# Performance work log

Measured on AMD Instinct MI355X. Metric: run time of the kernel, lower is better.

## Reference

```python
import jax, jax.numpy as jnp
import numpy as np

# --- hyperparameters (from MambaBlock init) ---
DIM = 256          # d_model per window
STEP = 128         # int(dim * hop), hop = 0.5
N_MAMBA = 2
D_STATE = 16
D_CONV = 4
EXPAND = 4
D_INNER = EXPAND * DIM          # 1024
DT_RANK = -(-DIM // 16)         # ceil(d_model/16) = 16
EPS = 1e-5
B_SZ = 4
T_LEN = 131072


def setup_inputs() -> dict:
    key = jax.random.key(0)
    ks = jax.random.split(key, 8)
    s = 0.02
    x = jax.random.normal(ks[0], (B_SZ, T_LEN), dtype=jnp.float32)
    in_proj_w = jax.random.normal(ks[1], (N_MAMBA, 2 * D_INNER, DIM), dtype=jnp.float32) * s
    conv_w = jax.random.normal(ks[2], (N_MAMBA, D_INNER, 1, D_CONV), dtype=jnp.float32) * 0.1
    conv_b = jnp.zeros((N_MAMBA, D_INNER), dtype=jnp.float32)
    x_proj_w = jax.random.normal(ks[3], (N_MAMBA, DT_RANK + 2 * D_STATE, D_INNER), dtype=jnp.float32) * s
    dt_std = DT_RANK ** -0.5
    dt_proj_w = jax.random.uniform(ks[4], (N_MAMBA, D_INNER, DT_RANK), minval=-dt_std, maxval=dt_std, dtype=jnp.float32)
    # dt bias: inverse-softplus of dt ~ LogUniform[1e-3, 0.1] (mamba_ssm init)
    dt = jnp.exp(jax.random.uniform(ks[5], (N_MAMBA, D_INNER), dtype=jnp.float32)
                 * (np.log(0.1) - np.log(1e-3)) + np.log(1e-3))
    dt_proj_b = dt + jnp.log(-jnp.expm1(-dt))
    A_log = jnp.log(jnp.broadcast_to(jnp.arange(1, D_STATE + 1, dtype=jnp.float32),
                                     (N_MAMBA, D_INNER, D_STATE)))
    D_param = jnp.ones((N_MAMBA, D_INNER), dtype=jnp.float32)
    out_proj_w = jax.random.normal(ks[6], (N_MAMBA, DIM, D_INNER), dtype=jnp.float32) * s
    norm_w = jnp.ones((N_MAMBA, DIM), dtype=jnp.float32)
    return dict(x=x, in_proj_w=in_proj_w, conv_w=conv_w, conv_b=conv_b,
                x_proj_w=x_proj_w, dt_proj_w=dt_proj_w, dt_proj_b=dt_proj_b,
                A_log=A_log, D_param=D_param, out_proj_w=out_proj_w, norm_w=norm_w)


def _rmsnorm(x, w):
    return x * jax.lax.rsqrt(jnp.mean(x * x, axis=-1, keepdims=True) + EPS) * w


def _selective_scan(u, delta, A, Bm, Cm, Dp):
    # u, delta: [B, L, Di]; A: [Di, N]; Bm, Cm: [B, L, N]; Dp: [Di]
    def step(h, inp):
        u_t, d_t, B_t, C_t = inp                       # [B,Di],[B,Di],[B,N],[B,N]
        dA = jnp.exp(d_t[:, :, None] * A)              # [B,Di,N]
        h = dA * h + (d_t * u_t)[:, :, None] * B_t[:, None, :]
        y_t = jnp.einsum('bdn,bn->bd', h, C_t)
        return h, y_t
    h0 = jnp.zeros((u.shape[0], u.shape[2], A.shape[1]), u.dtype)
    xs = (u.transpose(1, 0, 2), delta.transpose(1, 0, 2),
          Bm.transpose(1, 0, 2), Cm.transpose(1, 0, 2))
    _, ys = jax.lax.scan(step, h0, xs)                 # ys: [L, B, Di]
    return ys.transpose(1, 0, 2) + u * Dp


def _mamba(x, in_w, cw, cb, xp_w, dt_w, dt_b, A_log, Dp, out_w):
    # x: [B, L, d_model]
    xz = jnp.einsum('bld,ed->ble', x, in_w)            # [B, L, 2*Di]
    xc, z = jnp.split(xz, 2, axis=-1)
    # causal depthwise conv (torch pads d_conv-1 both sides then truncates to L)
    xc = xc.transpose(0, 2, 1)                         # [B, Di, L]
    xc = jax.lax.conv_general_dilated(xc, cw, window_strides=(1,),
                                      padding=[(D_CONV - 1, 0)],
                                      feature_group_count=D_INNER,
                                      dimension_numbers=('NCH', 'OIH', 'NCH'))
    xc = jax.nn.silu(xc + cb[None, :, None]).transpose(0, 2, 1)  # [B, L, Di]
    x_dbl = jnp.einsum('bld,ed->ble', xc, xp_w)        # [B, L, dt_rank + 2N]
    dt = x_dbl[..., :DT_RANK]
    Bm = x_dbl[..., DT_RANK:DT_RANK + D_STATE]
    Cm = x_dbl[..., DT_RANK + D_STATE:]
    delta = jax.nn.softplus(jnp.einsum('blr,dr->bld', dt, dt_w) + dt_b)
    A = -jnp.exp(A_log)                                # [Di, N]
    y = _selective_scan(xc, delta, A, Bm, Cm, Dp)
    y = y * jax.nn.silu(z)
    return jnp.einsum('bld,ed->ble', y, out_w)         # [B, L, d_model]


def _forward(x, in_proj_w, conv_w, conv_b, x_proj_w, dt_proj_w, dt_proj_b,
             A_log, D_param, out_proj_w, norm_w):
    B, T = x.shape
    L = (T - DIM) // STEP + 1
    idx = jnp.arange(L)[:, None] * STEP + jnp.arange(DIM)[None, :]  # [L, DIM]
    h = x[:, idx]                                      # unfold -> [B, L, DIM]
    res = None
    for i in range(N_MAMBA):
        res = h + res if res is not None else h        # Block residual chaining
        hn = _rmsnorm(res, norm_w[i])
        h = _mamba(hn, in_proj_w[i], conv_w[i], conv_b[i], x_proj_w[i],
                   dt_proj_w[i], dt_proj_b[i], A_log[i], D_param[i], out_proj_w[i])
    r = h + res
    # hop < 1: triangular window, then fold (overlap-add)
    half = DIM // 2
    win = jnp.concatenate([jnp.linspace(0.0, 1.0, half), jnp.linspace(1.0, 0.0, half)])
    r = r * win
    folded = jnp.zeros_like(x).at[:, idx].add(r)       # F.fold overlap-add
    return folded + x


def reference(x, in_proj_w, conv_w, conv_b, x_proj_w, dt_proj_w, dt_proj_b,
              A_log, D_param, out_proj_w, norm_w):
    return _forward(x, in_proj_w, conv_w, conv_b, x_proj_w, dt_proj_w, dt_proj_b,
                    A_log, D_param, out_proj_w, norm_w)
```

## Files before the change

### kernel.cpp

```cpp
#include <hip/hip_runtime.h>
#include <cmath>

#define DIMC   256
#define L_WIN  1023
#define M_VALID 4092
#define M_PAD  4096
#define DI     1024
#define TLEN   131072
#define SEG    32
#define NSEG   32

typedef __bf16 bf16x8 __attribute__((ext_vector_type(8)));
typedef __bf16 bf16x4 __attribute__((ext_vector_type(4)));
typedef float  f32x4  __attribute__((ext_vector_type(4)));

__device__ __forceinline__ float sigmoidf_(float x){ return 1.f/(1.f + __expf(-x)); }
__device__ __forceinline__ float softplusf_(float v){ return fmaxf(v,0.f) + log1pf(__expf(-fabsf(v))); }

template<int CTRL>
__device__ __forceinline__ float dpp_add(float x){
  int v = __builtin_amdgcn_update_dpp(0, __builtin_bit_cast(int, x), CTRL, 0xF, 0xF, true);
  return x + __builtin_bit_cast(float, v);
}

__global__ __launch_bounds__(256) void init_kernel(const float* __restrict__ x, float* __restrict__ res,
    const float* __restrict__ a, __bf16* __restrict__ da, int na,
    const float* __restrict__ b, __bf16* __restrict__ db, int nb,
    const float* __restrict__ c, __bf16* __restrict__ dc, int nc)
{
  if (blockIdx.x < M_PAD){
    int m = blockIdx.x, j = threadIdx.x;
    float v = 0.f;
    if (m < M_VALID){
      int bb = m / L_WIN, l = m - bb*L_WIN;
      v = x[(size_t)bb*TLEN + l*128 + j];
    }
    res[(size_t)m*DIMC + j] = v;
    return;
  }
  int nblk = gridDim.x - M_PAD;
  int stride = nblk*256;
  int base = (blockIdx.x - M_PAD)*256 + threadIdx.x;
  for (int i = base; i < na; i += stride) da[i] = (__bf16)a[i];
  for (int i = base; i < nb; i += stride) db[i] = (__bf16)b[i];
  for (int i = base; i < nc; i += stride) dc[i] = (__bf16)c[i];
}

__global__ __launch_bounds__(256) void rms_kernel(const float* __restrict__ src, __bf16* __restrict__ dst,
                                                  const float* __restrict__ w){
  int m = blockIdx.x, j = threadIdx.x;
  float v = (m < M_VALID) ? src[(size_t)m*DIMC + j] : 0.f;
  float s = v*v;
  #pragma unroll
  for (int off = 32; off; off >>= 1) s += __shfl_down(s, off);
  __shared__ float ls[4];
  if ((threadIdx.x & 63) == 0) ls[threadIdx.x >> 6] = s;
  __syncthreads();
  float tot = ls[0] + ls[1] + ls[2] + ls[3];
  float scale = rsqrtf(tot * (1.f/DIMC) + 1e-5f);
  dst[(size_t)m*DIMC + j] = (__bf16)(v * scale * w[j]);
}

template<int WM, int WN, typename OutT>
__global__ __launch_bounds__(256) void gemm_tiled_kernel(const __bf16* __restrict__ A, const __bf16* __restrict__ B,
    OutT* C, const float* addsrc, int K, int ldc)
{
  constexpr int BM  = 32*WM;
  constexpr int BN  = 32*WN;
  constexpr int LDK = 72;
  __shared__ __bf16 As[BM*LDK];
  __shared__ __bf16 Bs[BN*LDK];
  int tid  = threadIdx.x;
  int lane = tid & 63, wv = tid >> 6;
  int row  = lane & 15, kq = lane >> 4;
  int m0 = blockIdx.x*BM, n0 = blockIdx.y*BN;
  int wmo = (wv >> 1)*(16*WM);
  int wno = (wv &  1)*(16*WN);
  f32x4 acc[WM][WN] = {};
  for (int kt = 0; kt < K; kt += 64){
    __syncthreads();
    #pragma unroll
    for (int r = 0; r < BM/32; ++r){
      int seg = r*256 + tid;
      int rw = seg >> 3, sb = seg & 7;
      *(bf16x8*)(As + rw*LDK + sb*8) = *(const bf16x8*)(A + (size_t)(m0 + rw)*K + kt + sb*8);
    }
    #pragma unroll
    for (int r = 0; r < BN/32; ++r){
      int seg = r*256 + tid;
      int rw = seg >> 3, sb = seg & 7;
      *(bf16x8*)(Bs + rw*LDK + sb*8) = *(const bf16x8*)(B + (size_t)(n0 + rw)*K + kt + sb*8);
    }
    __syncthreads();
    #pragma unroll
    for (int ks = 0; ks < 2; ++ks){
      bf16x8 af[WM], bfr[WN];
      #pragma unroll
      for (int i = 0; i < WM; ++i) af[i]  = *(const bf16x8*)(As + (wmo + i*16 + row)*LDK + ks*32 + kq*8);
      #pragma unroll
      for (int j = 0; j < WN; ++j) bfr[j] = *(const bf16x8*)(Bs + (wno + j*16 + row)*LDK + ks*32 + kq*8);
      #pragma unroll
      for (int i = 0; i < WM; ++i){
        #pragma unroll
        for (int j = 0; j < WN; ++j)
          acc[i][j] = __builtin_amdgcn_mfma_f32_16x16x32_bf16(af[i], bfr[j], acc[i][j], 0, 0, 0);
      }
    }
  }
  #pragma unroll
  for (int i = 0; i < WM; ++i){
    int cm = m0 + wmo + i*16 + kq*4;
    #pragma unroll
    for (int j = 0; j < WN; ++j){
      int cn = n0 + wno + j*16 + row;
      #pragma unroll
      for (int ii = 0; ii < 4; ++ii){
        size_t idx = (size_t)(cm + ii)*ldc + cn;
        float v = acc[i][j][ii];
        if (addsrc) v += addsrc[idx];
        C[idx] = (OutT)v;
      }
    }
  }
}

template<int SUBN, typename OutT>
__global__ __launch_bounds__(256) void gemm_kernel(const __bf16* __restrict__ A, const __bf16* __restrict__ B,
    OutT* C, const float* addsrc, int K, int ldc)
{
  int lane = threadIdx.x & 63;
  int wv   = threadIdx.x >> 6;
  int row  = lane & 15;
  int kq   = lane >> 4;
  int m0 = blockIdx.x*64 + wv*16;
  int n0 = blockIdx.y*(16*SUBN);
  f32x4 acc[SUBN] = {};
  const __bf16* Ap = A + (size_t)(m0 + row)*K + kq*8;
  const __bf16* Bp = B + (size_t)(n0 + row)*K + kq*8;
  for (int k = 0; k < K; k += 32){
    bf16x8 a = *(const bf16x8*)(Ap + k);
    #pragma unroll
    for (int s = 0; s < SUBN; ++s){
      bf16x8 bb = *(const bf16x8*)(Bp + (size_t)s*16*K + k);
      acc[s] = __builtin_amdgcn_mfma_f32_16x16x32_bf16(a, bb, acc[s], 0, 0, 0);
    }
  }
  int cm = m0 + kq*4;
  #pragma unroll
  for (int s = 0; s < SUBN; ++s){
    int cn = n0 + s*16 + row;
    #pragma unroll
    for (int i = 0; i < 4; ++i){
      size_t idx = (size_t)(cm + i)*ldc + cn;
      float v = acc[s][i];
      if (addsrc) v += addsrc[idx];
      C[idx] = (OutT)v;
    }
  }
}

__global__ __launch_bounds__(256) void conv_kernel(const __bf16* __restrict__ xz16, const float* __restrict__ cw,
    const float* __restrict__ cb, __bf16* __restrict__ u16)
{
  int m0 = blockIdx.x * 16;
  int d  = threadIdx.x * 4;
  float w[4][4];
  #pragma unroll
  for (int c = 0; c < 4; ++c){
    #pragma unroll
    for (int j = 0; j < 4; ++j) w[c][j] = cw[(d + c)*4 + j];
  }
  float bias[4];
  #pragma unroll
  for (int c = 0; c < 4; ++c) bias[c] = cb[d + c];
  for (int ti = 0; ti < 16; ++ti){
    int m = m0 + ti;
    float acc[4] = {0.f, 0.f, 0.f, 0.f};
    if (m < M_VALID){
      int b = m / L_WIN;
      int l = m - b*L_WIN;
      #pragma unroll
      for (int c = 0; c < 4; ++c) acc[c] = bias[c];
      #pragma unroll
      for (int k = 0; k < 4; ++k){
        if (l >= k){
          bf16x4 xv = *(const bf16x4*)(xz16 + (size_t)(m - k)*2048 + d);
          #pragma unroll
          for (int c = 0; c < 4; ++c) acc[c] = fmaf((float)xv[c], w[c][3-k], acc[c]);
        }
      }
      #pragma unroll
      for (int c = 0; c < 4; ++c) acc[c] = acc[c] * sigmoidf_(acc[c]);
    }
    bf16x4 o;
    #pragma unroll
    for (int c = 0; c < 4; ++c) o[c] = (__bf16)acc[c];
    *(bf16x4*)(u16 + (size_t)m*DI + d) = o;
  }
}

__global__ __launch_bounds__(256) void dtproj_kernel(const float* __restrict__ xdbl, const float* __restrict__ dtw,
    const float* __restrict__ dtb, __bf16* __restrict__ delta16)
{
  int m0 = blockIdx.x * 16;
  int tid = threadIdx.x;
  __shared__ float sdt[16][17];
  sdt[tid >> 4][tid & 15] = xdbl[(size_t)(m0 + (tid >> 4))*48 + (tid & 15)];
  __syncthreads();
  int d0 = tid * 4;
  float w[4][16];
  #pragma unroll
  for (int c = 0; c < 4; ++c){
    #pragma unroll
    for (int q = 0; q < 16; ++q) w[c][q] = dtw[(d0 + c)*16 + q];
  }
  float bias[4];
  #pragma unroll
  for (int c = 0; c < 4; ++c) bias[c] = dtb[d0 + c];
  for (int t = 0; t < 16; ++t){
    float acc[4] = {bias[0], bias[1], bias[2], bias[3]};
    #pragma unroll
    for (int r = 0; r < 16; ++r){
      float dv = sdt[t][r];
      #pragma unroll
      for (int c = 0; c < 4; ++c) acc[c] = fmaf(dv, w[c][r], acc[c]);
    }
    bf16x4 o;
    #pragma unroll
    for (int c = 0; c < 4; ++c) o[c] = (__bf16)softplusf_(acc[c]);
    *(bf16x4*)(delta16 + (size_t)(m0 + t)*DI + d0) = o;
  }
}

__global__ __launch_bounds__(256) void scan_part1_kernel(
  const __bf16* __restrict__ u16, const __bf16* __restrict__ delta16,
  const float* __restrict__ xdbl, const float* __restrict__ Alog, float2* __restrict__ Pq)
{
  int bid = blockIdx.x;
  int s = bid & 31, dtile = (bid >> 5) & 63, b = bid >> 11;
  int d0 = dtile << 4;
  int tid = threadIdx.x;
  int c = tid >> 4, n = tid & 15;
  float A_dn = -__expf(Alog[(d0 + c)*16 + n]);
  __shared__ float2 sdd[16][SEG+2];
  __shared__ float  sB [SEG][17];
  int t0 = s*SEG;
  int nt = L_WIN - t0; if (nt > SEG) nt = SEG;
  size_t base_m = (size_t)b*L_WIN + t0;
  for (int i2 = tid; i2 < 16*SEG; i2 += 256){
    int tt = i2 >> 4, dd = i2 & 15;
    float dlt = 0.f, du = 0.f, Bv = 0.f;
    if (tt < nt){
      size_t m = base_m + tt;
      dlt = (float)delta16[m*DI + d0 + dd];
      du  = dlt * (float)u16[m*DI + d0 + dd];
      Bv  = xdbl[m*48 + 16 + dd];
    }
    sdd[dd][tt] = make_float2(dlt, du);
    sB[tt][dd]  = Bv;
  }
  __syncthreads();
  float h = 0.f, P = 1.f;
  #pragma unroll 8
  for (int t = 0; t < SEG; ++t){
    float2 dd2 = sdd[c][t];
    float dA = __expf(dd2.x * A_dn);
    h = fmaf(dA, h, dd2.y * sB[t][n]);
    P *= dA;
  }
  Pq[(((size_t)b*NSEG + s) << 14) + d0*16 + tid] = make_float2(P, h);
}

__global__ __launch_bounds__(256) void scan_combine_kernel(const float2* __restrict__ Pq,
                                                           float* __restrict__ hstart)
{
  int idx = blockIdx.x*256 + threadIdx.x;
  int b = idx >> 14;
  int dn = idx & 16383;
  float hs = 0.f;
  #pragma unroll
  for (int s = 0; s < NSEG; ++s){
    size_t o = (((size_t)b*NSEG + s) << 14) + dn;
    hstart[o] = hs;
    float2 pq = Pq[o];
    hs = fmaf(pq.x, hs, pq.y);
  }
}

__global__ __launch_bounds__(256) void scan_part2_kernel(
  const __bf16* __restrict__ u16, const __bf16* __restrict__ delta16,
  const float* __restrict__ xdbl, const __bf16* __restrict__ xz16,
  const float* __restrict__ Alog, const float* __restrict__ Dp,
  const float* __restrict__ hstart, __bf16* __restrict__ y16)
{
  int bid = blockIdx.x;
  int s = bid & 31, dtile = (bid >> 5) & 63, b = bid >> 11;
  int d0 = dtile << 4;
  int tid = threadIdx.x;
  int c = tid >> 4, n = tid & 15;
  float A_dn = -__expf(Alog[(d0 + c)*16 + n]);
  __shared__ float2 sdd[16][SEG+2];
  __shared__ float2 sBC[SEG][17];
  __shared__ float  sy [16][SEG+1];
  __shared__ float  sD[16];
  if (tid < 16) sD[tid] = Dp[d0 + tid];
  int t0 = s*SEG;
  int nt = L_WIN - t0; if (nt > SEG) nt = SEG;
  size_t base_m = (size_t)b*L_WIN + t0;
  for (int i2 = tid; i2 < 16*SEG; i2 += 256){
    int tt = i2 >> 4, dd = i2 & 15;
    float dlt = 0.f, uu = 0.f, Bv = 0.f, Cv = 0.f;
    if (tt < nt){
      size_t m = base_m + tt;
      dlt = (float)delta16[m*DI + d0 + dd];
      uu  = (float)u16[m*DI + d0 + dd];
      Bv  = xdbl[m*48 + 16 + dd];
      Cv  = xdbl[m*48 + 32 + dd];
    }
    sdd[dd][tt] = make_float2(dlt, uu);
    sBC[tt][dd] = make_float2(Bv, Cv);
  }
  float h = hstart[(((size_t)b*NSEG + s) << 14) + d0*16 + tid];
  __syncthreads();
  #pragma unroll 8
  for (int t = 0; t < SEG; ++t){
    float2 dd2 = sdd[c][t];
    float dA = __expf(dd2.x * A_dn);
    float2 bc = sBC[t][n];
    h = fmaf(dA, h, dd2.x * dd2.y * bc.x);
    float pp = h * bc.y;
    pp = dpp_add<0xB1>(pp);
    pp = dpp_add<0x4E>(pp);
    pp = dpp_add<0x141>(pp);
    pp = dpp_add<0x128>(pp);
    if (n == 0) sy[c][t] = pp;
  }
  __syncthreads();
  for (int i2 = tid; i2 < 16*nt; i2 += 256){
    int tt = i2 >> 4, dd = i2 & 15;
    size_t m = base_m + tt;
    float uv = sdd[dd][tt].y;
    float zv = (float)xz16[m*2048 + 1024 + d0 + dd];
    float yv = (sy[dd][tt] + uv * sD[dd]) * (zv * sigmoidf_(zv));
    y16[m*DI + d0 + dd] = (__bf16)yv;
  }
}

__global__ __launch_bounds__(256) void fold_kernel(const float* __restrict__ x, const float* __restrict__ r,
                                                   float* __restrict__ out){
  int i = blockIdx.x*256 + threadIdx.x;
  int b = i >> 17;
  int t = i & (TLEN - 1);
  float acc = x[i];
  int l1 = t >> 7;
  int j  = t & 127;
  if (l1 < L_WIN) acc += r[((size_t)b*L_WIN + l1)*DIMC + j] * ((float)j * (1.f/127.f));
  if (l1 >= 1)    acc += r[((size_t)b*L_WIN + l1 - 1)*DIMC + j + 128] * ((float)(127 - j) * (1.f/127.f));
  out[i] = acc;
}

extern "C" void kernel_launch(void* const* d_in, const int* in_sizes, int n_in,
                              void* d_out, int out_size, void* d_ws, size_t ws_size,
                              hipStream_t stream)
{
  (void)in_sizes; (void)n_in; (void)out_size; (void)ws_size;
  const float* x      = (const float*)d_in[0];
  const float* in_w   = (const float*)d_in[1];
  const float* conv_w = (const float*)d_in[2];
  const float* conv_b = (const float*)d_in[3];
  const float* xp_w   = (const float*)d_in[4];
  const float* dt_w   = (const float*)d_in[5];
  const float* dt_b   = (const float*)d_in[6];
  const float* A_log  = (const float*)d_in[7];
  const float* Dp     = (const float*)d_in[8];
  const float* out_w  = (const float*)d_in[9];
  const float* norm_w = (const float*)d_in[10];
  float* out = (float*)d_out;

  char* p = (char*)d_ws;
  auto alloc = [&](size_t bytes)->void*{ void* r = (void*)p; p += (bytes + 255) & ~(size_t)255; return r; };
  float*  res    = (float*) alloc((size_t)M_PAD*DIMC*4);
  __bf16* hn16   = (__bf16*)alloc((size_t)M_PAD*DIMC*2);
  __bf16* xz16   = (__bf16*)alloc((size_t)M_PAD*2048*2);
  __bf16* u16    = (__bf16*)alloc((size_t)M_PAD*DI*2);
  float*  xdbl   = (float*) alloc((size_t)M_PAD*48*4);
  __bf16* delta16= (__bf16*)alloc((size_t)M_PAD*DI*2);
  __bf16* y16    = (__bf16*)alloc((size_t)M_PAD*DI*2);
  float2* Pq     = (float2*)alloc((size_t)4*NSEG*16384*8);
  float*  hstart = (float*) alloc((size_t)4*NSEG*16384*4);
  __bf16* w_in16 = (__bf16*)alloc((size_t)2*2048*256*2);
  __bf16* w_xp16 = (__bf16*)alloc((size_t)2*48*1024*2);
  __bf16* w_out16= (__bf16*)alloc((size_t)2*256*1024*2);

  init_kernel<<<M_PAD + 512, 256, 0, stream>>>(x, res,
                                               in_w, w_in16, 2*2048*256,
                                               xp_w, w_xp16, 2*48*1024,
                                               out_w, w_out16, 2*256*1024);

  for (int i = 0; i < 2; ++i){
    rms_kernel<<<M_PAD, 256, 0, stream>>>(res, hn16, norm_w + i*256);
    gemm_tiled_kernel<4, 4, __bf16><<<dim3(32, 16), 256, 0, stream>>>(hn16, w_in16 + (size_t)i*524288, xz16, nullptr, 256, 2048);
    conv_kernel<<<M_PAD/16, 256, 0, stream>>>(xz16, conv_w + i*4096, conv_b + i*1024, u16);
    gemm_kernel<1, float><<<dim3(64, 3), 256, 0, stream>>>(u16, w_xp16 + (size_t)i*49152, xdbl, nullptr, 1024, 48);
    dtproj_kernel<<<M_PAD/16, 256, 0, stream>>>(xdbl, dt_w + i*16384, dt_b + i*1024, delta16);
    scan_part1_kernel<<<8192, 256, 0, stream>>>(u16, delta16, xdbl, A_log + i*16384, Pq);
    scan_combine_kernel<<<256, 256, 0, stream>>>(Pq, hstart);
    scan_part2_kernel<<<8192, 256, 0, stream>>>(u16, delta16, xdbl, xz16, A_log + i*16384, Dp + i*1024,
                                                hstart, y16);
    gemm_tiled_kernel<2, 2, float><<<dim3(64, 4), 256, 0, stream>>>(y16, w_out16 + (size_t)i*262144, res, res, 1024, 256);
  }
  fold_kernel<<<TLEN*4/256, 256, 0, stream>>>(x, res, out);
}
```

Measured before the change: 357.7 us.

## Fuse dt projection and three-pass selective scan into one block-per-chain kernel

Replaces the dt projection kernel and the three scan kernels (part1, combine, part2) with a single kernel. Each 1024-thread block owns one (batch, 16-channel) chain and walks the 32 segments in 8 rounds of 4, combining segment carries in shared memory. This removes the delta16, Pq and hstart global round-trips and three launches. The cost is that only 256 blocks run each scan, with sequential rounds and many barriers, so parallelism drops sharply compared with 8192 independent blocks. Delta and u are also now held at different precision (fp32 delta, bf16 u in shared memory).

```diff
diff --git a/kernel.cpp b/kernel.cpp
--- a/kernel.cpp
+++ b/kernel.cpp
@@ -9,6 +9,7 @@
 #define TLEN   131072
 #define SEG    32
 #define NSEG   32
+#define ROUNDS 8
 
 typedef __bf16 bf16x8 __attribute__((ext_vector_type(8)));
 typedef __bf16 bf16x4 __attribute__((ext_vector_type(4)));
@@ -199,150 +200,108 @@
   }
 }
 
-__global__ __launch_bounds__(256) void dtproj_kernel(const float* __restrict__ xdbl, const float* __restrict__ dtw,
-    const float* __restrict__ dtb, __bf16* __restrict__ delta16)
-{
-  int m0 = blockIdx.x * 16;
+__global__ __launch_bounds__(1024) void scan_fused_kernel(
+  const __bf16* __restrict__ u16, const float* __restrict__ xdbl,
+  const __bf16* __restrict__ xz16,
+  const float* __restrict__ dtw, const float* __restrict__ dtb,
+  const float* __restrict__ Alog, const float* __restrict__ Dp,
+  __bf16* __restrict__ y16)
+{
+  int chain = blockIdx.x;
+  int b = chain >> 6;
+  int d0 = (chain & 63) << 4;
   int tid = threadIdx.x;
-  __shared__ float sdt[16][17];
-  sdt[tid >> 4][tid & 15] = xdbl[(size_t)(m0 + (tid >> 4))*48 + (tid & 15)];
-  __syncthreads();
-  int d0 = tid * 4;
-  float w[4][16];
-  #pragma unroll
-  for (int c = 0; c < 4; ++c){
-    #pragma unroll
-    for (int q = 0; q < 16; ++q) w[c][q] = dtw[(d0 + c)*16 + q];
-  }
-  float bias[4];
-  #pragma unroll
-  for (int c = 0; c < 4; ++c) bias[c] = dtb[d0 + c];
-  for (int t = 0; t < 16; ++t){
-    float acc[4] = {bias[0], bias[1], bias[2], bias[3]};
-    #pragma unroll
-    for (int r = 0; r < 16; ++r){
-      float dv = sdt[t][r];
-      #pragma unroll
-      for (int c = 0; c < 4; ++c) acc[c] = fmaf(dv, w[c][r], acc[c]);
-    }
-    bf16x4 o;
-    #pragma unroll
-    for (int c = 0; c < 4; ++c) o[c] = (__bf16)softplusf_(acc[c]);
-    *(bf16x4*)(delta16 + (size_t)(m0 + t)*DI + d0) = o;
-  }
-}
-
-__global__ __launch_bounds__(256) void scan_part1_kernel(
-  const __bf16* __restrict__ u16, const __bf16* __restrict__ delta16,
-  const float* __restrict__ xdbl, const float* __restrict__ Alog, float2* __restrict__ Pq)
-{
-  int bid = blockIdx.x;
-  int s = bid & 31, dtile = (bid >> 5) & 63, b = bid >> 11;
-  int d0 = dtile << 4;
-  int tid = threadIdx.x;
-  int c = tid >> 4, n = tid & 15;
+  int g = tid >> 8;
+  int t256 = tid & 255;
+  int c = t256 >> 4, n = t256 & 15;
   float A_dn = -__expf(Alog[(d0 + c)*16 + n]);
-  __shared__ float2 sdd[16][SEG+2];
-  __shared__ float  sB [SEG][17];
-  int t0 = s*SEG;
-  int nt = L_WIN - t0; if (nt > SEG) nt = SEG;
-  size_t base_m = (size_t)b*L_WIN + t0;
-  for (int i2 = tid; i2 < 16*SEG; i2 += 256){
-    int tt = i2 >> 4, dd = i2 & 15;
-    float dlt = 0.f, du = 0.f, Bv = 0.f;
-    if (tt < nt){
+
+  __shared__ float2 sdd[4][16][SEG+1];
+  __shared__ float2 sBC[4][SEG][17];
+  __shared__ float  sy [4][16][SEG+1];
+  __shared__ __bf16 su [4][16][SEG+2];
+  __shared__ float  sdt[4][SEG][17];
+  __shared__ float2 strans[4][256];
+  __shared__ float  sH[2][256];
+  __shared__ float  sW[16][17];
+  __shared__ float  sbias[16];
+  __shared__ float  sD[16];
+
+  if (tid < 256){
+    sW[c][n] = dtw[(size_t)(d0 + c)*16 + n];
+    sH[0][t256] = 0.f;
+    if (tid < 16){ sbias[tid] = dtb[d0 + tid]; sD[tid] = Dp[d0 + tid]; }
+  }
+
+  for (int r = 0; r < ROUNDS; ++r){
+    int s = r*4 + g;
+    int t0 = s*SEG;
+    int nt = L_WIN - t0; if (nt > SEG) nt = SEG;
+    size_t base_m = (size_t)b*L_WIN + t0;
+    __syncthreads();
+    for (int i2 = t256; i2 < 16*SEG; i2 += 256){
+      int tt = i2 >> 4, k = i2 & 15;
+      float dtv = 0.f, Bv = 0.f, Cv = 0.f, uu = 0.f;
+      if (tt < nt){
+        const float* rowp = xdbl + (base_m + tt)*48;
+        dtv = rowp[k]; Bv = rowp[16 + k]; Cv = rowp[32 + k];
+        uu  = (float)u16[(base_m + tt)*DI + d0 + k];
+      }
+      sdt[g][tt][k] = dtv;
+      sBC[g][tt][k] = make_float2(Bv, Cv);
+      su[g][k][tt]  = (__bf16)uu;
+    }
+    __syncthreads();
+    for (int i2 = t256; i2 < 16*SEG; i2 += 256){
+      int tt = i2 >> 4, dd = i2 & 15;
+      float acc = sbias[dd];
+      #pragma unroll
+      for (int rr = 0; rr < 16; ++rr) acc = fmaf(sdt[g][tt][rr], sW[dd][rr], acc);
+      float dlt = softplusf_(acc);
+      float uu = (float)su[g][dd][tt];
+      sdd[g][dd][tt] = make_float2(dlt, dlt * uu);
+    }
+    __syncthreads();
+    float h = 0.f, P = 1.f;
+    #pragma unroll 8
+    for (int t = 0; t < SEG; ++t){
+      float2 d2 = sdd[g][c][t];
+      float dA = __expf(d2.x * A_dn);
+      h = fmaf(dA, h, d2.y * sBC[g][t][n].x);
+      P *= dA;
+    }
+    strans[g][t256] = make_float2(P, h);
+    __syncthreads();
+    int par = r & 1;
+    float hs = sH[par][t256];
+    #pragma unroll
+    for (int k = 0; k < 3; ++k){
+      if (k < g){ float2 tr = strans[k][t256]; hs = fmaf(tr.x, hs, tr.y); }
+    }
+    if (g == 3){ float2 tr = strans[3][t256]; sH[par ^ 1][t256] = fmaf(tr.x, hs, tr.y); }
+    h = hs;
+    #pragma unroll 8
+    for (int t = 0; t < SEG; ++t){
+      float2 d2 = sdd[g][c][t];
+      float dA = __expf(d2.x * A_dn);
+      float2 bc = sBC[g][t][n];
+      h = fmaf(dA, h, d2.y * bc.x);
+      float pp = h * bc.y;
+      pp = dpp_add<0xB1>(pp);
+      pp = dpp_add<0x4E>(pp);
+      pp = dpp_add<0x141>(pp);
+      pp = dpp_add<0x128>(pp);
+      if (n == 0) sy[g][c][t] = pp;
+    }
+    __syncthreads();
+    for (int i2 = t256; i2 < 16*nt; i2 += 256){
+      int tt = i2 >> 4, dd = i2 & 15;
       size_t m = base_m + tt;
-      dlt = (float)delta16[m*DI + d0 + dd];
-      du  = dlt * (float)u16[m*DI + d0 + dd];
-      Bv  = xdbl[m*48 + 16 + dd];
-    }
-    sdd[dd][tt] = make_float2(dlt, du);
-    sB[tt][dd]  = Bv;
-  }
-  __syncthreads();
-  float h = 0.f, P = 1.f;
-  #pragma unroll 8
-  for (int t = 0; t < SEG; ++t){
-    float2 dd2 = sdd[c][t];
-    float dA = __expf(dd2.x * A_dn);
-    h = fmaf(dA, h, dd2.y * sB[t][n]);
-    P *= dA;
-  }
-  Pq[(((size_t)b*NSEG + s) << 14) + d0*16 + tid] = make_float2(P, h);
-}
-
-__global__ __launch_bounds__(256) void scan_combine_kernel(const float2* __restrict__ Pq,
-                                                           float* __restrict__ hstart)
-{
-  int idx = blockIdx.x*256 + threadIdx.x;
-  int b = idx >> 14;
-  int dn = idx & 16383;
-  float hs = 0.f;
-  #pragma unroll
-  for (int s = 0; s < NSEG; ++s){
-    size_t o = (((size_t)b*NSEG + s) << 14) + dn;
-    hstart[o] = hs;
-    float2 pq = Pq[o];
-    hs = fmaf(pq.x, hs, pq.y);
-  }
-}
-
-__global__ __launch_bounds__(256) void scan_part2_kernel(
-  const __bf16* __restrict__ u16, const __bf16* __restrict__ delta16,
-  const float* __restrict__ xdbl, const __bf16* __restrict__ xz16,
-  const float* __restrict__ Alog, const float* __restrict__ Dp,
-  const float* __restrict__ hstart, __bf16* __restrict__ y16)
-{
-  int bid = blockIdx.x;
-  int s = bid & 31, dtile = (bid >> 5) & 63, b = bid >> 11;
-  int d0 = dtile << 4;
-  int tid = threadIdx.x;
-  int c = tid >> 4, n = tid & 15;
-  float A_dn = -__expf(Alog[(d0 + c)*16 + n]);
-  __shared__ float2 sdd[16][SEG+2];
-  __shared__ float2 sBC[SEG][17];
-  __shared__ float  sy [16][SEG+1];
-  __shared__ float  sD[16];
-  if (tid < 16) sD[tid] = Dp[d0 + tid];
-  int t0 = s*SEG;
-  int nt = L_WIN - t0; if (nt > SEG) nt = SEG;
-  size_t base_m = (size_t)b*L_WIN + t0;
-  for (int i2 = tid; i2 < 16*SEG; i2 += 256){
-    int tt = i2 >> 4, dd = i2 & 15;
-    float dlt = 0.f, uu = 0.f, Bv = 0.f, Cv = 0.f;
-    if (tt < nt){
-      size_t m = base_m + tt;
-      dlt = (float)delta16[m*DI + d0 + dd];
-      uu  = (float)u16[m*DI + d0 + dd];
-      Bv  = xdbl[m*48 + 16 + dd];
-      Cv  = xdbl[m*48 + 32 + dd];
-    }
-    sdd[dd][tt] = make_float2(dlt, uu);
-    sBC[tt][dd] = make_float2(Bv, Cv);
-  }
-  float h = hstart[(((size_t)b*NSEG + s) << 14) + d0*16 + tid];
-  __syncthreads();
-  #pragma unroll 8
-  for (int t = 0; t < SEG; ++t){
-    float2 dd2 = sdd[c][t];
-    float dA = __expf(dd2.x * A_dn);
-    float2 bc = sBC[t][n];
-    h = fmaf(dA, h, dd2.x * dd2.y * bc.x);
-    float pp = h * bc.y;
-    pp = dpp_add<0xB1>(pp);
-    pp = dpp_add<0x4E>(pp);
-    pp = dpp_add<0x141>(pp);
-    pp = dpp_add<0x128>(pp);
-    if (n == 0) sy[c][t] = pp;
-  }
-  __syncthreads();
-  for (int i2 = tid; i2 < 16*nt; i2 += 256){
-    int tt = i2 >> 4, dd = i2 & 15;
-    size_t m = base_m + tt;
-    float uv = sdd[dd][tt].y;
-    float zv = (float)xz16[m*2048 + 1024 + d0 + dd];
-    float yv = (sy[dd][tt] + uv * sD[dd]) * (zv * sigmoidf_(zv));
-    y16[m*DI + d0 + dd] = (__bf16)yv;
+      float uv = (float)su[g][dd][tt];
+      float zv = (float)xz16[m*2048 + 1024 + d0 + dd];
+      float yv = (sy[g][dd][tt] + uv * sD[dd]) * (zv * sigmoidf_(zv));
+      y16[m*DI + d0 + dd] = (__bf16)yv;
+    }
   }
 }
 
@@ -384,10 +343,7 @@
   __bf16* xz16   = (__bf16*)alloc((size_t)M_PAD*2048*2);
   __bf16* u16    = (__bf16*)alloc((size_t)M_PAD*DI*2);
   float*  xdbl   = (float*) alloc((size_t)M_PAD*48*4);
-  __bf16* delta16= (__bf16*)alloc((size_t)M_PAD*DI*2);
   __bf16* y16    = (__bf16*)alloc((size_t)M_PAD*DI*2);
-  float2* Pq     = (float2*)alloc((size_t)4*NSEG*16384*8);
-  float*  hstart = (float*) alloc((size_t)4*NSEG*16384*4);
   __bf16* w_in16 = (__bf16*)alloc((size_t)2*2048*256*2);
   __bf16* w_xp16 = (__bf16*)alloc((size_t)2*48*1024*2);
   __bf16* w_out16= (__bf16*)alloc((size_t)2*256*1024*2);
@@ -402,11 +358,8 @@
     gemm_tiled_kernel<4, 4, __bf16><<<dim3(32, 16), 256, 0, stream>>>(hn16, w_in16 + (size_t)i*524288, xz16, nullptr, 256, 2048);
     conv_kernel<<<M_PAD/16, 256, 0, stream>>>(xz16, conv_w + i*4096, conv_b + i*1024, u16);
     gemm_kernel<1, float><<<dim3(64, 3), 256, 0, stream>>>(u16, w_xp16 + (size_t)i*49152, xdbl, nullptr, 1024, 48);
-    dtproj_kernel<<<M_PAD/16, 256, 0, stream>>>(xdbl, dt_w + i*16384, dt_b + i*1024, delta16);
-    scan_part1_kernel<<<8192, 256, 0, stream>>>(u16, delta16, xdbl, A_log + i*16384, Pq);
-    scan_combine_kernel<<<256, 256, 0, stream>>>(Pq, hstart);
-    scan_part2_kernel<<<8192, 256, 0, stream>>>(u16, delta16, xdbl, xz16, A_log + i*16384, Dp + i*1024,
-                                                hstart, y16);
+    scan_fused_kernel<<<256, 1024, 0, stream>>>(u16, xdbl, xz16, dt_w + i*16384, dt_b + i*1024,
+                                                A_log + i*16384, Dp + i*1024, y16);
     gemm_tiled_kernel<2, 2, float><<<dim3(64, 4), 256, 0, stream>>>(y16, w_out16 + (size_t)i*262144, res, res, 1024, 256);
   }
   fold_kernel<<<TLEN*4/256, 256, 0, stream>>>(x, res, out);
```

Measured after the change: 370.7 us. +3.6%, slower.

## Fuse conv, x_proj GEMM and dt_proj into one kernel per token tile

Applied to the files above, without the earlier changes.

Merges the depthwise conv+SiLU, the x_proj GEMM and the dt_proj+softplus into a single kernel working on 16-token tiles. The conv output is staged in shared memory and fed straight to MFMA for x_proj, and the dt rows pass through shared memory to dt_proj. This removes two launches and the global re-reads of u16 and xdbl. In exchange, only 3 of 4 waves do the x_proj GEMM, there are extra barriers, and each block streams the full x_proj weight.

```diff
diff --git a/kernel.cpp b/kernel.cpp
--- a/kernel.cpp
+++ b/kernel.cpp
@@ -124,111 +124,93 @@
   }
 }
 
-template<int SUBN, typename OutT>
-__global__ __launch_bounds__(256) void gemm_kernel(const __bf16* __restrict__ A, const __bf16* __restrict__ B,
-    OutT* C, const float* addsrc, int K, int ldc)
-{
-  int lane = threadIdx.x & 63;
-  int wv   = threadIdx.x >> 6;
-  int row  = lane & 15;
-  int kq   = lane >> 4;
-  int m0 = blockIdx.x*64 + wv*16;
-  int n0 = blockIdx.y*(16*SUBN);
-  f32x4 acc[SUBN] = {};
-  const __bf16* Ap = A + (size_t)(m0 + row)*K + kq*8;
-  const __bf16* Bp = B + (size_t)(n0 + row)*K + kq*8;
-  for (int k = 0; k < K; k += 32){
-    bf16x8 a = *(const bf16x8*)(Ap + k);
-    #pragma unroll
-    for (int s = 0; s < SUBN; ++s){
-      bf16x8 bb = *(const bf16x8*)(Bp + (size_t)s*16*K + k);
-      acc[s] = __builtin_amdgcn_mfma_f32_16x16x32_bf16(a, bb, acc[s], 0, 0, 0);
-    }
-  }
-  int cm = m0 + kq*4;
-  #pragma unroll
-  for (int s = 0; s < SUBN; ++s){
-    int cn = n0 + s*16 + row;
-    #pragma unroll
-    for (int i = 0; i < 4; ++i){
-      size_t idx = (size_t)(cm + i)*ldc + cn;
-      float v = acc[s][i];
-      if (addsrc) v += addsrc[idx];
-      C[idx] = (OutT)v;
-    }
-  }
-}
-
-__global__ __launch_bounds__(256) void conv_kernel(const __bf16* __restrict__ xz16, const float* __restrict__ cw,
-    const float* __restrict__ cb, __bf16* __restrict__ u16)
-{
+__global__ __launch_bounds__(256) void conv_xproj_dt_kernel(
+  const __bf16* __restrict__ xz16, const float* __restrict__ cw, const float* __restrict__ cb,
+  const __bf16* __restrict__ wxp, const float* __restrict__ dtw, const float* __restrict__ dtb,
+  __bf16* __restrict__ u16, float* __restrict__ xdbl, __bf16* __restrict__ delta16)
+{
+  __shared__ __bf16 su[16][1032];
+  __shared__ float  sdt[16][17];
+  int tid = threadIdx.x;
   int m0 = blockIdx.x * 16;
-  int d  = threadIdx.x * 4;
-  float w[4][4];
-  #pragma unroll
-  for (int c = 0; c < 4; ++c){
-    #pragma unroll
-    for (int j = 0; j < 4; ++j) w[c][j] = cw[(d + c)*4 + j];
-  }
-  float bias[4];
-  #pragma unroll
-  for (int c = 0; c < 4; ++c) bias[c] = cb[d + c];
-  for (int ti = 0; ti < 16; ++ti){
-    int m = m0 + ti;
-    float acc[4] = {0.f, 0.f, 0.f, 0.f};
-    if (m < M_VALID){
-      int b = m / L_WIN;
-      int l = m - b*L_WIN;
-      #pragma unroll
-      for (int c = 0; c < 4; ++c) acc[c] = bias[c];
-      #pragma unroll
-      for (int k = 0; k < 4; ++k){
-        if (l >= k){
-          bf16x4 xv = *(const bf16x4*)(xz16 + (size_t)(m - k)*2048 + d);
-          #pragma unroll
-          for (int c = 0; c < 4; ++c) acc[c] = fmaf((float)xv[c], w[c][3-k], acc[c]);
+  {
+    int d = tid * 4;
+    float w[4][4], bias[4];
+    #pragma unroll
+    for (int c = 0; c < 4; ++c){
+      #pragma unroll
+      for (int j = 0; j < 4; ++j) w[c][j] = cw[(d + c)*4 + j];
+      bias[c] = cb[d + c];
+    }
+    for (int ti = 0; ti < 16; ++ti){
+      int m = m0 + ti;
+      float acc[4] = {0.f, 0.f, 0.f, 0.f};
+      if (m < M_VALID){
+        int b = m / L_WIN;
+        int l = m - b*L_WIN;
+        #pragma unroll
+        for (int c = 0; c < 4; ++c) acc[c] = bias[c];
+        #pragma unroll
+        for (int k = 0; k < 4; ++k){
+          if (l >= k){
+            bf16x4 xv = *(const bf16x4*)(xz16 + (size_t)(m - k)*2048 + d);
+            #pragma unroll
+            for (int c = 0; c < 4; ++c) acc[c] = fmaf((float)xv[c], w[c][3-k], acc[c]);
+          }
         }
-      }
-      #pragma unroll
-      for (int c = 0; c < 4; ++c) acc[c] = acc[c] * sigmoidf_(acc[c]);
-    }
-    bf16x4 o;
-    #pragma unroll
-    for (int c = 0; c < 4; ++c) o[c] = (__bf16)acc[c];
-    *(bf16x4*)(u16 + (size_t)m*DI + d) = o;
-  }
-}
-
-__global__ __launch_bounds__(256) void dtproj_kernel(const float* __restrict__ xdbl, const float* __restrict__ dtw,
-    const float* __restrict__ dtb, __bf16* __restrict__ delta16)
-{
-  int m0 = blockIdx.x * 16;
-  int tid = threadIdx.x;
-  __shared__ float sdt[16][17];
-  sdt[tid >> 4][tid & 15] = xdbl[(size_t)(m0 + (tid >> 4))*48 + (tid & 15)];
-  __syncthreads();
-  int d0 = tid * 4;
-  float w[4][16];
-  #pragma unroll
-  for (int c = 0; c < 4; ++c){
-    #pragma unroll
-    for (int q = 0; q < 16; ++q) w[c][q] = dtw[(d0 + c)*16 + q];
-  }
-  float bias[4];
-  #pragma unroll
-  for (int c = 0; c < 4; ++c) bias[c] = dtb[d0 + c];
-  for (int t = 0; t < 16; ++t){
-    float acc[4] = {bias[0], bias[1], bias[2], bias[3]};
-    #pragma unroll
-    for (int r = 0; r < 16; ++r){
-      float dv = sdt[t][r];
-      #pragma unroll
-      for (int c = 0; c < 4; ++c) acc[c] = fmaf(dv, w[c][r], acc[c]);
-    }
-    bf16x4 o;
-    #pragma unroll
-    for (int c = 0; c < 4; ++c) o[c] = (__bf16)softplusf_(acc[c]);
-    *(bf16x4*)(delta16 + (size_t)(m0 + t)*DI + d0) = o;
+        #pragma unroll
+        for (int c = 0; c < 4; ++c) acc[c] = acc[c] * sigmoidf_(acc[c]);
+      }
+      bf16x4 o;
+      #pragma unroll
+      for (int c = 0; c < 4; ++c) o[c] = (__bf16)acc[c];
+      *(bf16x4*)(u16 + (size_t)m*DI + d) = o;
+      *(bf16x4*)(&su[ti][d]) = o;
+    }
+  }
+  __syncthreads();
+  {
+    int lane = tid & 63, wv = tid >> 6;
+    if (wv < 3){
+      int row = lane & 15, kq = lane >> 4;
+      f32x4 acc = {0.f, 0.f, 0.f, 0.f};
+      const __bf16* Bp = wxp + (size_t)(wv*16 + row)*1024 + kq*8;
+      for (int k = 0; k < 1024; k += 32){
+        bf16x8 a  = *(const bf16x8*)(&su[row][k + kq*8]);
+        bf16x8 bb = *(const bf16x8*)(Bp + k);
+        acc = __builtin_amdgcn_mfma_f32_16x16x32_bf16(a, bb, acc, 0, 0, 0);
+      }
+      #pragma unroll
+      for (int i = 0; i < 4; ++i){
+        int tok = kq*4 + i;
+        xdbl[(size_t)(m0 + tok)*48 + wv*16 + row] = acc[i];
+        if (wv == 0) sdt[tok][row] = acc[i];
+      }
+    }
+  }
+  __syncthreads();
+  {
+    int d0 = tid * 4;
+    float w[4][16], bias[4];
+    #pragma unroll
+    for (int c = 0; c < 4; ++c){
+      #pragma unroll
+      for (int q = 0; q < 16; ++q) w[c][q] = dtw[(d0 + c)*16 + q];
+      bias[c] = dtb[d0 + c];
+    }
+    for (int t = 0; t < 16; ++t){
+      float acc[4] = {bias[0], bias[1], bias[2], bias[3]};
+      #pragma unroll
+      for (int r = 0; r < 16; ++r){
+        float dv = sdt[t][r];
+        #pragma unroll
+        for (int c = 0; c < 4; ++c) acc[c] = fmaf(dv, w[c][r], acc[c]);
+      }
+      bf16x4 o;
+      #pragma unroll
+      for (int c = 0; c < 4; ++c) o[c] = (__bf16)softplusf_(acc[c]);
+      *(bf16x4*)(delta16 + (size_t)(m0 + t)*DI + d0) = o;
+    }
   }
 }
 
@@ -400,9 +382,9 @@
   for (int i = 0; i < 2; ++i){
     rms_kernel<<<M_PAD, 256, 0, stream>>>(res, hn16, norm_w + i*256);
     gemm_tiled_kernel<4, 4, __bf16><<<dim3(32, 16), 256, 0, stream>>>(hn16, w_in16 + (size_t)i*524288, xz16, nullptr, 256, 2048);
-    conv_kernel<<<M_PAD/16, 256, 0, stream>>>(xz16, conv_w + i*4096, conv_b + i*1024, u16);
-    gemm_kernel<1, float><<<dim3(64, 3), 256, 0, stream>>>(u16, w_xp16 + (size_t)i*49152, xdbl, nullptr, 1024, 48);
-    dtproj_kernel<<<M_PAD/16, 256, 0, stream>>>(xdbl, dt_w + i*16384, dt_b + i*1024, delta16);
+    conv_xproj_dt_kernel<<<M_PAD/16, 256, 0, stream>>>(xz16, conv_w + i*4096, conv_b + i*1024,
+                                                       w_xp16 + (size_t)i*49152, dt_w + i*16384, dt_b + i*1024,
+                                                       u16, xdbl, delta16);
     scan_part1_kernel<<<8192, 256, 0, stream>>>(u16, delta16, xdbl, A_log + i*16384, Pq);
     scan_combine_kernel<<<256, 256, 0, stream>>>(Pq, hstart);
     scan_part2_kernel<<<8192, 256, 0, stream>>>(u16, delta16, xdbl, xz16, A_log + i*16384, Dp + i*1024,
```

After: 339.4 us, median of 2. 1.05x faster.
